# Kernel tuning notes

Measured on AMD Instinct MI355X. Metric: run time of the kernel, lower is better.

Reference implementation:

```python
import jax, jax.numpy as jnp
import numpy as np

B, K, D = 64, 2048, 32400  # batch, num bases, in_features**2 (180*180)


def setup_inputs() -> dict:
    key = jax.random.key(0)
    k1, k2, k3, k4, k5, k6 = jax.random.split(key, 6)
    s = 1.0 / np.sqrt(K)  # matches uniform(-sqrt(1/K), sqrt(1/K)) scale of weight init
    return {
        "X_re": jax.random.normal(k1, (B, D), dtype=jnp.float32),
        "X_im": jax.random.normal(k2, (B, D), dtype=jnp.float32),
        "bases_re": jax.random.normal(k3, (K, D), dtype=jnp.float32) * 0.004,
        "bases_im": jax.random.normal(k4, (K, D), dtype=jnp.float32) * 0.004,
        "weight_re": jax.random.normal(k5, (K,), dtype=jnp.float32) * s,
        "weight_im": jax.random.normal(k6, (K,), dtype=jnp.float32) * s,
    }


def reference(X_re, X_im, bases_re, bases_im, weight_re, weight_im):
    # Assemble complex64 operands
    X = jax.lax.complex(X_re, X_im)          # [B, D]
    bases = jax.lax.complex(bases_re, bases_im)  # [K, D]
    w = jax.lax.complex(weight_re, weight_im)    # [K]
    # X @ conj(bases)^T -> [B, K]; diag_embed(weight) matmul == per-basis scale
    coeffs = jnp.matmul(X, jnp.conj(bases).T) * w[None, :]
    # project back: [B, K] @ [K, D] -> [B, D]
    out = jnp.matmul(coeffs, bases)
    # complex->channels->complex round trip in the original is the identity
    return out
```

## Files before the change

kernel.cpp:

```cpp
#include <hip/hip_runtime.h>
#include <hip/hip_bf16.h>
#include <cstdint>
#include <cstddef>

#define B_DIM 64
#define K_DIM 2048
#define D_DIM 32400

typedef __bf16 bf16x8 __attribute__((ext_vector_type(8)));
typedef float f32x4 __attribute__((ext_vector_type(4)));

union U128 { uint4 u; bf16x8 b; };

__device__ inline bf16x8 asbf(uint4 u) { U128 x; x.u = u; return x.b; }

__device__ inline uint4 neg4(uint4 u) {
    u.x ^= 0x80008000u; u.y ^= 0x80008000u; u.z ^= 0x80008000u; u.w ^= 0x80008000u;
    return u;
}

__device__ inline f32x4 mfma16(bf16x8 a, bf16x8 b, f32x4 c) {
    return __builtin_amdgcn_mfma_f32_16x16x32_bf16(a, b, c, 0, 0, 0);
}

__device__ inline f32x4 ld4g(const float* __restrict__ p, int d, int dlim) {
    f32x4 r;
    if (d + 4 <= dlim) {
        float4 v = *reinterpret_cast<const float4*>(p + d);
        r[0] = v.x; r[1] = v.y; r[2] = v.z; r[3] = v.w;
    } else {
        #pragma unroll
        for (int j = 0; j < 4; ++j) r[j] = (d + j < dlim) ? p[d + j] : 0.0f;
    }
    return r;
}

__device__ inline uint32_t pk(float a, float b) {
    union { __bf16 h[2]; uint32_t u; } x;
    x.h[0] = (__bf16)a; x.h[1] = (__bf16)b;
    return x.u;
}

#define P1_STRIDE 72

__global__ __launch_bounds__(256) void p1_coeffs(
    const float* __restrict__ Xre, const float* __restrict__ Xim,
    const float* __restrict__ Bre, const float* __restrict__ Bim,
    const float* __restrict__ Wre, const float* __restrict__ Wim,
    float* __restrict__ Cre, float* __restrict__ Cim)
{
    __shared__ __align__(16) __bf16 sX[2][2][64][P1_STRIDE];
    __shared__ __align__(16) __bf16 sB[2][2][64][P1_STRIDE];

    const int dc = blockIdx.x;
    const int kt = blockIdx.y;
    const int tid  = threadIdx.x;
    const int lane = tid & 63;
    const int w    = tid >> 6;
    const int r    = lane & 15;
    const int g    = lane >> 4;

    const int kbase  = kt * 64;
    const int dstart = dc * 1024;
    const int dend   = min(dstart + 1024, D_DIM);
    const int nsteps = (dend - dstart + 63) >> 6;

    const int srow = tid >> 2;
    const int sc   = (tid & 3) * 4;

    const size_t xo = (size_t)srow * D_DIM;
    const size_t bo = (size_t)(kbase + srow) * D_DIM;

    f32x4 st[16];

    auto LOADS = [&](int s) {
        const int dg = dstart + s * 64 + sc;
        #pragma unroll
        for (int j = 0; j < 4; ++j) st[j]      = ld4g(Xre + xo, dg + j * 16, dend);
        #pragma unroll
        for (int j = 0; j < 4; ++j) st[4 + j]  = ld4g(Xim + xo, dg + j * 16, dend);
        #pragma unroll
        for (int j = 0; j < 4; ++j) st[8 + j]  = ld4g(Bre + bo, dg + j * 16, dend);
        #pragma unroll
        for (int j = 0; j < 4; ++j) st[12 + j] = ld4g(Bim + bo, dg + j * 16, dend);
    };

    auto WRITE = [&](int buf) {
        #pragma unroll
        for (int j = 0; j < 4; ++j) {
            const int dp = sc + j * 16;
            *(uint2*)&sX[buf][0][srow][dp] = make_uint2(pk(st[j][0],      st[j][1]),      pk(st[j][2],      st[j][3]));
            *(uint2*)&sX[buf][1][srow][dp] = make_uint2(pk(st[4 + j][0],  st[4 + j][1]),  pk(st[4 + j][2],  st[4 + j][3]));
            *(uint2*)&sB[buf][0][srow][dp] = make_uint2(pk(st[8 + j][0],  st[8 + j][1]),  pk(st[8 + j][2],  st[8 + j][3]));
            *(uint2*)&sB[buf][1][srow][dp] = make_uint2(pk(st[12 + j][0], st[12 + j][1]), pk(st[12 + j][2], st[12 + j][3]));
        }
    };

    const int m0  = (w & 1) * 32;
    const int nl0 = (w >> 1) * 32;

    f32x4 accRe[2][2] = {};
    f32x4 accIm[2][2] = {};

    auto COMPUTE = [&](int buf) {
        #pragma unroll
        for (int kk = 0; kk < 2; ++kk) {
            const int dp = kk * 32 + g * 8;
            uint4 xre[2], xim[2], bre[2], bim[2];
            #pragma unroll
            for (int ms = 0; ms < 2; ++ms) {
                xre[ms] = *(const uint4*)&sX[buf][0][m0 + ms * 16 + r][dp];
                xim[ms] = *(const uint4*)&sX[buf][1][m0 + ms * 16 + r][dp];
            }
            #pragma unroll
            for (int ns = 0; ns < 2; ++ns) {
                bre[ns] = *(const uint4*)&sB[buf][0][nl0 + ns * 16 + r][dp];
                bim[ns] = *(const uint4*)&sB[buf][1][nl0 + ns * 16 + r][dp];
            }
            #pragma unroll
            for (int ms = 0; ms < 2; ++ms)
            #pragma unroll
            for (int ns = 0; ns < 2; ++ns) {
                accRe[ms][ns] = mfma16(asbf(xre[ms]), asbf(bre[ns]), accRe[ms][ns]);
                accRe[ms][ns] = mfma16(asbf(xim[ms]), asbf(bim[ns]), accRe[ms][ns]);
                accIm[ms][ns] = mfma16(asbf(xim[ms]), asbf(bre[ns]), accIm[ms][ns]);
                accIm[ms][ns] = mfma16(asbf(neg4(xre[ms])), asbf(bim[ns]), accIm[ms][ns]);
            }
        }
    };

    LOADS(0); WRITE(0); __syncthreads();
    for (int s = 0; s < nsteps; ++s) {
        if (s + 1 < nsteps) LOADS(s + 1);
        COMPUTE(s & 1);
        if (s + 1 < nsteps) WRITE((s + 1) & 1);
        __syncthreads();
    }

    #pragma unroll
    for (int ms = 0; ms < 2; ++ms)
    #pragma unroll
    for (int ns = 0; ns < 2; ++ns) {
        const int kb = kbase + nl0 + ns * 16 + r;
        const float wre = Wre[kb], wim = Wim[kb];
        #pragma unroll
        for (int i = 0; i < 4; ++i) {
            const int b = m0 + ms * 16 + g * 4 + i;
            const float cre = accRe[ms][ns][i];
            const float cim = accIm[ms][ns][i];
            atomicAdd(&Cre[b * K_DIM + kb], cre * wre - cim * wim);
            atomicAdd(&Cim[b * K_DIM + kb], cre * wim + cim * wre);
        }
    }
}

__global__ __launch_bounds__(256) void cbf_kernel(
    const float* __restrict__ Cre, const float* __restrict__ Cim,
    __bf16* __restrict__ CreBf, __bf16* __restrict__ CimBf)
{
    const int i = blockIdx.x * 256 + threadIdx.x;
    if (i < B_DIM * K_DIM) {
        CreBf[i] = (__bf16)Cre[i];
        CimBf[i] = (__bf16)Cim[i];
    }
}

#define P2_STRIDE 72

template <bool WIM>
__global__ __launch_bounds__(256) void p2_project(
    const float* __restrict__ Bre, const float* __restrict__ Bim,
    const __bf16* __restrict__ CreBf, const __bf16* __restrict__ CimBf,
    float* __restrict__ out)
{
    __shared__ __align__(16) __bf16 sT[2][2][64][P2_STRIDE];

    const int dt = blockIdx.x;
    const int kh = blockIdx.y;
    const int d0 = dt * 64;
    const int khbase = kh * (K_DIM / 2);
    const int tid  = threadIdx.x;
    const int lane = tid & 63;
    const int w    = tid >> 6;
    const int r    = lane & 15;
    const int g    = lane >> 4;

    const int kq = tid >> 4;
    const int ds = (tid & 15) * 4;

    f32x4 st[8];

    auto LOADS = [&](int t) {
        const int k0 = khbase + t * 64;
        #pragma unroll
        for (int j = 0; j < 4; ++j) {
            const size_t ro = (size_t)(k0 + kq * 4 + j) * D_DIM;
            st[j]     = ld4g(Bre + ro, d0 + ds, D_DIM);
            st[4 + j] = ld4g(Bim + ro, d0 + ds, D_DIM);
        }
    };

    auto WRITE = [&](int buf) {
        #pragma unroll
        for (int i = 0; i < 4; ++i) {
            *(uint2*)&sT[buf][0][ds + i][kq * 4] =
                make_uint2(pk(st[0][i], st[1][i]), pk(st[2][i], st[3][i]));
            *(uint2*)&sT[buf][1][ds + i][kq * 4] =
                make_uint2(pk(st[4][i], st[5][i]), pk(st[6][i], st[7][i]));
        }
    };

    const int m0  = (w & 1) * 32;
    const int nl0 = (w >> 1) * 32;

    f32x4 accRe[2][2] = {};
    f32x4 accIm[2][2] = {};

    auto COMPUTE = [&](int t, int buf) {
        const int k0 = khbase + t * 64;
        uint4 aRe[2][2], aIm[2][2];
        #pragma unroll
        for (int ms = 0; ms < 2; ++ms) {
            const size_t rowo = (size_t)(m0 + ms * 16 + r) * K_DIM;
            #pragma unroll
            for (int kk = 0; kk < 2; ++kk) {
                aRe[ms][kk] = *(const uint4*)&CreBf[rowo + k0 + kk * 32 + g * 8];
                aIm[ms][kk] = *(const uint4*)&CimBf[rowo + k0 + kk * 32 + g * 8];
            }
        }
        #pragma unroll
        for (int kk = 0; kk < 2; ++kk) {
            uint4 bre[2], bim[2];
            #pragma unroll
            for (int ns = 0; ns < 2; ++ns) {
                bre[ns] = *(const uint4*)&sT[buf][0][nl0 + ns * 16 + r][kk * 32 + g * 8];
                bim[ns] = *(const uint4*)&sT[buf][1][nl0 + ns * 16 + r][kk * 32 + g * 8];
            }
            #pragma unroll
            for (int ms = 0; ms < 2; ++ms)
            #pragma unroll
            for (int ns = 0; ns < 2; ++ns) {
                accRe[ms][ns] = mfma16(asbf(aRe[ms][kk]), asbf(bre[ns]), accRe[ms][ns]);
                accRe[ms][ns] = mfma16(asbf(neg4(aIm[ms][kk])), asbf(bim[ns]), accRe[ms][ns]);
                if (WIM) {
                    accIm[ms][ns] = mfma16(asbf(aRe[ms][kk]), asbf(bim[ns]), accIm[ms][ns]);
                    accIm[ms][ns] = mfma16(asbf(aIm[ms][kk]), asbf(bre[ns]), accIm[ms][ns]);
                }
            }
        }
    };

    const int NT = (K_DIM / 2) / 64;
    LOADS(0); WRITE(0); __syncthreads();
    for (int t = 0; t < NT; ++t) {
        if (t + 1 < NT) LOADS(t + 1);
        COMPUTE(t, t & 1);
        if (t + 1 < NT) WRITE((t + 1) & 1);
        __syncthreads();
    }

    #pragma unroll
    for (int ms = 0; ms < 2; ++ms)
    #pragma unroll
    for (int ns = 0; ns < 2; ++ns) {
        const int d = d0 + nl0 + ns * 16 + r;
        if (d < D_DIM) {
            #pragma unroll
            for (int i = 0; i < 4; ++i) {
                const int b = m0 + ms * 16 + g * 4 + i;
                if (!WIM) {
                    atomicAdd(&out[(size_t)b * D_DIM + d], accRe[ms][ns][i]);
                } else {
                    atomicAdd(&out[((size_t)b * D_DIM + d) * 2],     accRe[ms][ns][i]);
                    atomicAdd(&out[((size_t)b * D_DIM + d) * 2 + 1], accIm[ms][ns][i]);
                }
            }
        }
    }
}

extern "C" void kernel_launch(void* const* d_in, const int* in_sizes, int n_in,
                              void* d_out, int out_size, void* d_ws, size_t ws_size,
                              hipStream_t stream) {
    const float* Xre = (const float*)d_in[0];
    const float* Xim = (const float*)d_in[1];
    const float* Bre = (const float*)d_in[2];
    const float* Bim = (const float*)d_in[3];
    const float* Wre = (const float*)d_in[4];
    const float* Wim = (const float*)d_in[5];

    float*  Cre   = (float*)d_ws;
    float*  Cim   = Cre + B_DIM * K_DIM;
    __bf16* CreBf = (__bf16*)(Cim + B_DIM * K_DIM);
    __bf16* CimBf = CreBf + B_DIM * K_DIM;

    (void)hipMemsetAsync(d_ws, 0, (size_t)2 * B_DIM * K_DIM * sizeof(float), stream);
    (void)hipMemsetAsync(d_out, 0, (size_t)out_size * sizeof(float), stream);

    dim3 g1(32, 32);
    p1_coeffs<<<g1, 256, 0, stream>>>(Xre, Xim, Bre, Bim, Wre, Wim, Cre, Cim);

    cbf_kernel<<<(B_DIM * K_DIM + 255) / 256, 256, 0, stream>>>(Cre, Cim, CreBf, CimBf);

    const int ndt = (D_DIM + 63) / 64;
    dim3 g2(ndt, 2);
    if (out_size == 2 * B_DIM * D_DIM) {
        p2_project<true><<<g2, 256, 0, stream>>>(Bre, Bim, CreBf, CimBf, (float*)d_out);
    } else {
        p2_project<false><<<g2, 256, 0, stream>>>(Bre, Bim, CreBf, CimBf, (float*)d_out);
    }
}
```

Baseline: 331.2 us.

## Coalesce phase-1 global loads, single-buffer LDS, and swap grid axes

Each thread now loads from four rows at one 16-byte column position, so sixteen consecutive threads cover 256 contiguous bytes of a row. Before, four threads covered one row with 16-element strides. LDS drops from double to single buffering, halving shared memory to allow more resident blocks, at the cost of an extra barrier per step. The grid axes are swapped so consecutive blocks share the same D chunk across different K tiles, which should improve L2 reuse of X.

```diff
diff --git a/kernel.cpp b/kernel.cpp
--- a/kernel.cpp
+++ b/kernel.cpp
@@ -49,11 +49,11 @@
     const float* __restrict__ Wre, const float* __restrict__ Wim,
     float* __restrict__ Cre, float* __restrict__ Cim)
 {
-    __shared__ __align__(16) __bf16 sX[2][2][64][P1_STRIDE];
-    __shared__ __align__(16) __bf16 sB[2][2][64][P1_STRIDE];
-
-    const int dc = blockIdx.x;
-    const int kt = blockIdx.y;
+    __shared__ __align__(16) __bf16 sX[2][64][P1_STRIDE];
+    __shared__ __align__(16) __bf16 sB[2][64][P1_STRIDE];
+
+    const int kt = blockIdx.x;
+    const int dc = blockIdx.y;
     const int tid  = threadIdx.x;
     const int lane = tid & 63;
     const int w    = tid >> 6;
@@ -65,34 +65,31 @@
     const int dend   = min(dstart + 1024, D_DIM);
     const int nsteps = (dend - dstart + 63) >> 6;
 
-    const int srow = tid >> 2;
-    const int sc   = (tid & 3) * 4;
-
-    const size_t xo = (size_t)srow * D_DIM;
-    const size_t bo = (size_t)(kbase + srow) * D_DIM;
+    const int srow = tid >> 4;
+    const int sd   = (tid & 15) * 4;
 
     f32x4 st[16];
 
     auto LOADS = [&](int s) {
-        const int dg = dstart + s * 64 + sc;
-        #pragma unroll
-        for (int j = 0; j < 4; ++j) st[j]      = ld4g(Xre + xo, dg + j * 16, dend);
-        #pragma unroll
-        for (int j = 0; j < 4; ++j) st[4 + j]  = ld4g(Xim + xo, dg + j * 16, dend);
-        #pragma unroll
-        for (int j = 0; j < 4; ++j) st[8 + j]  = ld4g(Bre + bo, dg + j * 16, dend);
-        #pragma unroll
-        for (int j = 0; j < 4; ++j) st[12 + j] = ld4g(Bim + bo, dg + j * 16, dend);
-    };
-
-    auto WRITE = [&](int buf) {
+        const int dg = dstart + s * 64 + sd;
         #pragma unroll
         for (int j = 0; j < 4; ++j) {
-            const int dp = sc + j * 16;
-            *(uint2*)&sX[buf][0][srow][dp] = make_uint2(pk(st[j][0],      st[j][1]),      pk(st[j][2],      st[j][3]));
-            *(uint2*)&sX[buf][1][srow][dp] = make_uint2(pk(st[4 + j][0],  st[4 + j][1]),  pk(st[4 + j][2],  st[4 + j][3]));
-            *(uint2*)&sB[buf][0][srow][dp] = make_uint2(pk(st[8 + j][0],  st[8 + j][1]),  pk(st[8 + j][2],  st[8 + j][3]));
-            *(uint2*)&sB[buf][1][srow][dp] = make_uint2(pk(st[12 + j][0], st[12 + j][1]), pk(st[12 + j][2], st[12 + j][3]));
+            const int row = j * 16 + srow;
+            st[j]      = ld4g(Xre + (size_t)row * D_DIM, dg, dend);
+            st[4 + j]  = ld4g(Xim + (size_t)row * D_DIM, dg, dend);
+            st[8 + j]  = ld4g(Bre + (size_t)(kbase + row) * D_DIM, dg, dend);
+            st[12 + j] = ld4g(Bim + (size_t)(kbase + row) * D_DIM, dg, dend);
+        }
+    };
+
+    auto WRITE = [&]() {
+        #pragma unroll
+        for (int j = 0; j < 4; ++j) {
+            const int row = j * 16 + srow;
+            *(uint2*)&sX[0][row][sd] = make_uint2(pk(st[j][0],      st[j][1]),      pk(st[j][2],      st[j][3]));
+            *(uint2*)&sX[1][row][sd] = make_uint2(pk(st[4 + j][0],  st[4 + j][1]),  pk(st[4 + j][2],  st[4 + j][3]));
+            *(uint2*)&sB[0][row][sd] = make_uint2(pk(st[8 + j][0],  st[8 + j][1]),  pk(st[8 + j][2],  st[8 + j][3]));
+            *(uint2*)&sB[1][row][sd] = make_uint2(pk(st[12 + j][0], st[12 + j][1]), pk(st[12 + j][2], st[12 + j][3]));
         }
     };
 
@@ -102,20 +99,20 @@
     f32x4 accRe[2][2] = {};
     f32x4 accIm[2][2] = {};
 
-    auto COMPUTE = [&](int buf) {
+    auto COMPUTE = [&]() {
         #pragma unroll
         for (int kk = 0; kk < 2; ++kk) {
             const int dp = kk * 32 + g * 8;
             uint4 xre[2], xim[2], bre[2], bim[2];
             #pragma unroll
             for (int ms = 0; ms < 2; ++ms) {
-                xre[ms] = *(const uint4*)&sX[buf][0][m0 + ms * 16 + r][dp];
-                xim[ms] = *(const uint4*)&sX[buf][1][m0 + ms * 16 + r][dp];
+                xre[ms] = *(const uint4*)&sX[0][m0 + ms * 16 + r][dp];
+                xim[ms] = *(const uint4*)&sX[1][m0 + ms * 16 + r][dp];
             }
             #pragma unroll
             for (int ns = 0; ns < 2; ++ns) {
-                bre[ns] = *(const uint4*)&sB[buf][0][nl0 + ns * 16 + r][dp];
-                bim[ns] = *(const uint4*)&sB[buf][1][nl0 + ns * 16 + r][dp];
+                bre[ns] = *(const uint4*)&sB[0][nl0 + ns * 16 + r][dp];
+                bim[ns] = *(const uint4*)&sB[1][nl0 + ns * 16 + r][dp];
             }
             #pragma unroll
             for (int ms = 0; ms < 2; ++ms)
@@ -129,12 +126,15 @@
         }
     };
 
-    LOADS(0); WRITE(0); __syncthreads();
+    LOADS(0); WRITE(); __syncthreads();
     for (int s = 0; s < nsteps; ++s) {
         if (s + 1 < nsteps) LOADS(s + 1);
-        COMPUTE(s & 1);
-        if (s + 1 < nsteps) WRITE((s + 1) & 1);
-        __syncthreads();
+        COMPUTE();
+        if (s + 1 < nsteps) {
+            __syncthreads();
+            WRITE();
+            __syncthreads();
+        }
     }
 
     #pragma unroll
```

Measured after the change: 325.6 us. No clear change (-1.7%).
